# Optimization experiments

Measured on AMD Instinct MI355X. Metric: run time of the kernel, lower is better.

## Reference

```python
import jax, jax.numpy as jnp
import numpy as np
import math

B, S, D, H = 2, 1024, 4096, 32
HD = D // H          # head_dim = 128
P = 10               # prompt_len
THETA = 500000.0     # rope_theta


def _rope(t, cos, sin):
    # t: [b, s, h, hd]; pairs (2i, 2i+1) form complex numbers as in view_as_complex
    tr = t[..., 0::2]
    ti = t[..., 1::2]
    c = cos[None, :, None, :]
    s = sin[None, :, None, :]
    out = jnp.stack([tr * c - ti * s, tr * s + ti * c], axis=-1)  # [b,s,h,hd/2,2]
    return out.reshape(t.shape)


def setup_inputs() -> dict:
    key = jax.random.key(0)
    ks = jax.random.split(key, 8)
    sc = 0.02
    x = jax.random.normal(ks[0], (B, S, D), jnp.float32)
    wq = jax.random.normal(ks[1], (D, D), jnp.float32) * sc
    wk = jax.random.normal(ks[2], (D, D), jnp.float32) * sc
    wv = jax.random.normal(ks[3], (D, D), jnp.float32) * sc
    wo = jax.random.normal(ks[4], (D, D), jnp.float32) * sc
    prompt = jax.random.normal(ks[5], (P, D), jnp.float32)
    prompt_gate = jax.random.normal(ks[6], (1, H, 1, 1), jnp.float32) * 0.1
    # RoPE tables (real/imag of freqs_cis)
    inv = 1.0 / (THETA ** (jnp.arange(0, HD, 2, dtype=jnp.float32) / HD))  # [HD/2]
    ang = jnp.outer(jnp.arange(S, dtype=jnp.float32), inv)                 # [S, HD/2]
    freqs_cos = jnp.cos(ang)
    freqs_sin = jnp.sin(ang)
    # causal additive mask
    mask = jnp.triu(jnp.full((S, S), -1e9, jnp.float32), 1)[None, None]
    type_weight = jax.random.uniform(ks[7], (B, S, 1), jnp.float32)
    return dict(x=x, wq=wq, wk=wk, wv=wv, wo=wo, prompt=prompt,
                prompt_gate=prompt_gate, freqs_cos=freqs_cos,
                freqs_sin=freqs_sin, mask=mask, type_weight=type_weight,
                start_pos=0)


def reference(x, wq, wk, wv, wo, prompt, prompt_gate, freqs_cos, freqs_sin,
              mask, type_weight, start_pos):
    # training-mode forward: start_pos == 0, keys/values = current tokens
    scale = 1.0 / math.sqrt(HD)
    xq = (x @ wq.T).reshape(B, S, H, HD)
    xk = (x @ wk.T).reshape(B, S, H, HD)
    xv = (x @ wv.T).reshape(B, S, H, HD)
    xq = _rope(xq, freqs_cos, freqs_sin)
    xk = _rope(xk, freqs_cos, freqs_sin)
    q = xq.transpose(0, 2, 1, 3)  # [b,h,s,hd]
    k = xk.transpose(0, 2, 1, 3)
    v = xv.transpose(0, 2, 1, 3)
    scores = jnp.einsum('bhqd,bhkd->bhqk', q, k) * scale + mask
    probs = jax.nn.softmax(scores, axis=-1)
    out = jnp.einsum('bhqk,bhkd->bhqd', probs, v)  # [b,h,s,hd]
    # gated prompt injection (num_experts == 1); type_weight unused, as in source
    pk = (prompt @ wk.T).reshape(P, H, HD)
    pv = (prompt @ wv.T).reshape(P, H, HD)
    p_scores = jnp.einsum('bhqd,phd->bhqp', q, pk) * scale
    p_probs = prompt_gate * jax.nn.softmax(p_scores, axis=-1)
    p_out = jnp.einsum('bhqp,phd->bhqd', p_probs, pv)
    out = (out + p_out).transpose(0, 2, 1, 3).reshape(B, S, D)
    return out @ wo.T
```

## Files before the change

### kernel.cpp

```cpp
#include <hip/hip_runtime.h>
#include <hip/hip_bf16.h>
#include <stdint.h>

typedef __hip_bfloat16 bf16;
typedef __attribute__((ext_vector_type(8))) short short8;
typedef __attribute__((ext_vector_type(4))) float f32x4;

#define SCALE_ 0.08838834764831845f

static __device__ __forceinline__ float bf2f(short u) {
  unsigned int x = ((unsigned int)(unsigned short)u) << 16;
  return __builtin_bit_cast(float, x);
}
static __device__ __forceinline__ short f2bf(float f) {
  __hip_bfloat16 h = __float2bfloat16(f);
  return __builtin_bit_cast(short, h);
}
static __device__ __forceinline__ f32x4 mfma16(short8 a, short8 b, f32x4 c) {
  return __builtin_amdgcn_mfma_f32_16x16x32_bf16(a, b, c, 0, 0, 0);
}
static __device__ __forceinline__ void gl_lds16(const bf16* g, bf16* l) {
  __builtin_amdgcn_global_load_lds(
      (const __attribute__((address_space(1))) unsigned int*)g,
      (__attribute__((address_space(3))) unsigned int*)l, 16, 0, 0);
}

__global__ __launch_bounds__(256) void cvt6(
    const float* __restrict__ sx, const float* __restrict__ sq,
    const float* __restrict__ sk, const float* __restrict__ sv,
    const float* __restrict__ so, const float* __restrict__ sp,
    bf16* __restrict__ dx, bf16* __restrict__ dq, bf16* __restrict__ dk,
    bf16* __restrict__ dv, bf16* __restrict__ d4, bf16* __restrict__ dp)
{
  int b = blockIdx.x;
  const float* s; bf16* d; int off;
  if (b < 4096)       { s = sx; d = dx; off = b; }
  else if (b < 12288) { s = sq; d = dq; off = b - 4096; }
  else if (b < 20480) { s = sk; d = dk; off = b - 12288; }
  else if (b < 28672) { s = sv; d = dv; off = b - 20480; }
  else if (b < 36864) { s = so; d = d4; off = b - 28672; }
  else                { s = sp; d = dp; off = b - 36864; }
  long base = (long)off * 2048 + threadIdx.x * 8;
  f32x4 a = *(const f32x4*)(s + base);
  f32x4 c = *(const f32x4*)(s + base + 4);
  short8 o;
#pragma unroll
  for (int j = 0; j < 4; j++) { o[j] = f2bf(a[j]); o[4 + j] = f2bf(c[j]); }
  *(short8*)(d + base) = o;
}

template <int NKT, bool KSPLIT>
__global__ __launch_bounds__(512, 2) void gemm_bt(
    const bf16* __restrict__ A, const bf16* __restrict__ A2,
    const bf16* __restrict__ B0, const bf16* __restrict__ B1, const bf16* __restrict__ B2w,
    bf16* __restrict__ C0, bf16* __restrict__ C1, bf16* __restrict__ C2,
    bf16* __restrict__ P1, bf16* __restrict__ P2,
    float* __restrict__ CF,
    int M1, int Mtot)
{
  __shared__ char lds[131072];
  const int tid = threadIdx.x, w = tid >> 6, l = tid & 63;
  const int lr = l & 15, lg = l >> 4;
  const int wm = w >> 2, wn = w & 3;
  const int z = blockIdx.z;
  const bf16* Bw = KSPLIT ? B0 : ((z == 0) ? B0 : ((z == 1) ? B1 : B2w));
  bf16* C  = (z == 0) ? C0 : ((z == 1) ? C1 : C2);
  bf16* Cp = (KSPLIT || z == 0) ? (bf16*)0 : ((z == 1) ? P1 : P2);
  float* CFz = CF;
  long koff = 0;
  if (KSPLIT) { koff = (long)z * NKT * 64; CFz = CF + (long)z * M1 * 4096; }

  const int cpx = gridDim.x >> 3, orig = blockIdx.x;
  const int wg = (orig & 7) * cpx + (orig >> 3);
  const long m0 = (long)(wg >> 4) * 256;
  const long n0 = (long)(wg & 15) * 256;

  const int r0 = ((tid >> 3) << 1) | ((tid >> 2) & 1);
  const int c0 = (tid & 3) ^ ((tid >> 3) & 3);
  const bf16 *pa0, *pa1;
  {
    long mx = (long)(Mtot - M1) - 1;
    long g0 = m0 + r0, g1 = m0 + r0 + 128;
    const bf16 *q0, *q1;
    if (g0 < M1) q0 = A + g0 * 4096;
    else { long rr = g0 - M1; if (rr > mx) rr = mx; q0 = A2 + rr * 4096; }
    if (g1 < M1) q1 = A + g1 * 4096;
    else { long rr = g1 - M1; if (rr > mx) rr = mx; q1 = A2 + rr * 4096; }
    pa0 = q0 + c0 * 8 + koff;
    pa1 = q1 + c0 * 8 + koff;
  }
  const bf16* pb0 = Bw + (n0 + r0) * 4096 + c0 * 8 + koff;
  const bf16* pb1 = pb0 + (long)128 * 4096;

  const int ro  = (lr >> 1) * 128 + (((lr & 1) * 4) + (lg ^ ((lr >> 1) & 3))) * 16;
  const int aro = wm * 8192 + ro;
  const int bro = wn * 4096 + ro;

  f32x4 acc[8][4];
#pragma unroll
  for (int i = 0; i < 8; i++)
#pragma unroll
    for (int j = 0; j < 4; j++) acc[i][j] = (f32x4){0.f, 0.f, 0.f, 0.f};

  short8 af[4], bf[4];

#define STGA(S_, KE_)                                                        \
  {                                                                          \
    bf16* d_ = (bf16*)(lds + (S_) * 16384) + tid * 8;                        \
    gl_lds16(pa0 + (KE_), d_);                                               \
    gl_lds16(pa1 + (KE_), d_ + 4096);                                        \
  }
#define STGB(S_, KE_)                                                        \
  {                                                                          \
    bf16* d_ = (bf16*)(lds + (S_) * 16384) + tid * 8;                        \
    gl_lds16(pb0 + (KE_), d_);                                               \
    gl_lds16(pb1 + (KE_), d_ + 4096);                                        \
  }
#define SYNC(VM_)                                                            \
  {                                                                          \
    asm volatile("s_waitcnt vmcnt(" VM_ ")" ::: "memory");                   \
    __builtin_amdgcn_s_barrier();                                            \
    __builtin_amdgcn_sched_barrier(0);                                       \
  }
#define PHASE(PRB_, AU_, BU_, MO_, LB_, STG_)                                \
  {                                                                          \
    STG_                                                                     \
    const char* ab_ = lds + (PRB_) + (AU_) + aro;                            \
    _Pragma("unroll") for (int mi = 0; mi < 4; mi++)                         \
      af[mi] = *(const short8*)(ab_ + ((MO_) + mi) * 1024);                  \
    if (LB_) {                                                               \
      const char* bb_ = lds + (PRB_) + (BU_) + bro;                          \
      _Pragma("unroll") for (int ni = 0; ni < 4; ni++)                       \
        bf[ni] = *(const short8*)(bb_ + ni * 1024);                          \
    }                                                                        \
    asm volatile("s_waitcnt lgkmcnt(0)" ::: "memory");                       \
    __builtin_amdgcn_sched_barrier(0);                                       \
    __builtin_amdgcn_s_setprio(1);                                           \
    _Pragma("unroll") for (int mi = 0; mi < 4; mi++)                         \
      _Pragma("unroll") for (int ni = 0; ni < 4; ni++)                       \
        acc[(MO_) + mi][ni] = mfma16(af[mi], bf[ni], acc[(MO_) + mi][ni]);   \
    __builtin_amdgcn_s_setprio(0);                                           \
  }
#define KT(PRB_, S6_, S7_, S8_, S9_, KE1_, KE2_)                             \
  SYNC("8") PHASE(PRB_, 0, 16384, 0, 1, STGA(S6_, KE1_))                     \
  PHASE(PRB_, 0, 16384, 4, 0, STGB(S7_, KE1_))                               \
  SYNC("8") PHASE(PRB_, 32768, 49152, 0, 1, STGA(S8_, KE2_))                 \
  PHASE(PRB_, 32768, 49152, 4, 0, STGB(S9_, KE2_))

  STGA(0, 0) STGB(1, 0) STGA(2, 32) STGB(3, 32) STGA(4, 64) STGB(5, 64)

  for (int t = 0; t < NKT - 2; t += 2) {
    const int ka = (t + 1) * 64 + 32, kb = (t + 2) * 64;
    const int kc = (t + 2) * 64 + 32, kd = (t + 3) * 64;
    KT(0, 6, 7, 0, 1, ka, kb)
    KT(65536, 2, 3, 4, 5, kc, kd)
  }
  {
    const int kel = (NKT - 1) * 64 + 32;
    SYNC("8") PHASE(0, 0, 16384, 0, 1, STGA(6, kel))
    PHASE(0, 0, 16384, 4, 0, STGB(7, kel))
    SYNC("8") PHASE(0, 32768, 49152, 0, 1, )
    PHASE(0, 32768, 49152, 4, 0, )
  }
  SYNC("4") PHASE(65536, 0, 16384, 0, 1, )
  PHASE(65536, 0, 16384, 4, 0, )
  SYNC("0") PHASE(65536, 32768, 49152, 0, 1, )
  PHASE(65536, 32768, 49152, 4, 0, )

#undef KT
#undef PHASE
#undef SYNC
#undef STGB
#undef STGA

#pragma unroll
  for (int mi = 0; mi < 8; mi++) {
#pragma unroll
    for (int ni = 0; ni < 4; ni++) {
      long col = n0 + wn * 64 + ni * 16 + lr;
      f32x4 v = acc[mi][ni];
#pragma unroll
      for (int j = 0; j < 4; j++) {
        long row = m0 + wm * 128 + mi * 16 + lg * 4 + j;
        if (CFz) {
          CFz[row * 4096 + col] = v[j];
        } else if (row < M1) {
          *(short*)(C + row * 4096 + col) = f2bf(v[j]);
        } else if (Cp != 0 && row < Mtot) {
          *(short*)(Cp + (row - M1) * 4096 + col) = f2bf(v[j]);
        }
      }
    }
  }
}

__global__ __launch_bounds__(512, 2) void gemm_n128(
    const bf16* __restrict__ A, const bf16* __restrict__ Bw,
    float* __restrict__ CF)
{
  __shared__ char lds[98304];
  const int tid = threadIdx.x, w = tid >> 6, l = tid & 63;
  const int lr = l & 15, lg = l >> 4;
  const int wm = w >> 1, wn = w & 1;

  const int cpx = gridDim.x >> 3, orig = blockIdx.x;
  const int wg = (orig & 7) * cpx + (orig >> 3);
  const long m0 = (long)(wg >> 5) * 256;
  const long n0 = (long)(wg & 31) * 128;

  const int r0 = ((tid >> 3) << 1) | ((tid >> 2) & 1);
  const int c0 = (tid & 3) ^ ((tid >> 3) & 3);
  const bf16* pa0 = A + (m0 + r0) * 4096 + c0 * 8;
  const bf16* pa1 = pa0 + (long)128 * 4096;
  const bf16* pb0 = Bw + (n0 + r0) * 4096 + c0 * 8;

  const int ro  = (lr >> 1) * 128 + (((lr & 1) * 4) + (lg ^ ((lr >> 1) & 3))) * 16;
  const int aro = wm * 4096 + ro;
  const int bro = wn * 4096 + ro;

  f32x4 acc[4][4];
#pragma unroll
  for (int i = 0; i < 4; i++)
#pragma unroll
    for (int j = 0; j < 4; j++) acc[i][j] = (f32x4){0.f, 0.f, 0.f, 0.f};

  short8 af[4], bf[4];

#define NSTGA(SB_, KE_)                                                      \
  {                                                                          \
    bf16* d_ = (bf16*)(lds + (SB_)) + tid * 8;                               \
    gl_lds16(pa0 + (KE_), d_);                                               \
    gl_lds16(pa1 + (KE_), d_ + 4096);                                        \
  }
#define NSTGB(SB_, KE_)                                                      \
  {                                                                          \
    bf16* d_ = (bf16*)(lds + (SB_)) + tid * 8;                               \
    gl_lds16(pb0 + (KE_), d_);                                               \
  }
#define NSYNC(VM_)                                                           \
  {                                                                          \
    asm volatile("s_waitcnt vmcnt(" VM_ ")" ::: "memory");                   \
    __builtin_amdgcn_s_barrier();                                            \
    __builtin_amdgcn_sched_barrier(0);                                       \
  }
#define NPH(PRB_, AO_, BO_, STG_)                                            \
  {                                                                          \
    STG_                                                                     \
    const char* ab_ = lds + (PRB_) + (AO_) + aro;                            \
    _Pragma("unroll") for (int mi = 0; mi < 4; mi++)                         \
      af[mi] = *(const short8*)(ab_ + mi * 1024);                            \
    const char* bb_ = lds + (PRB_) + (BO_) + bro;                            \
    _Pragma("unroll") for (int ni = 0; ni < 4; ni++)                         \
      bf[ni] = *(const short8*)(bb_ + ni * 1024);                            \
    asm volatile("s_waitcnt lgkmcnt(0)" ::: "memory");                       \
    __builtin_amdgcn_sched_barrier(0);                                       \
    __builtin_amdgcn_s_setprio(1);                                           \
    _Pragma("unroll") for (int mi = 0; mi < 4; mi++)                         \
      _Pragma("unroll") for (int ni = 0; ni < 4; ni++)                       \
        acc[mi][ni] = mfma16(af[mi], bf[ni], acc[mi][ni]);                   \
    __builtin_amdgcn_s_setprio(0);                                           \
  }

  NSTGA(0, 0)      NSTGB(16384, 0)
  NSTGA(24576, 32) NSTGB(40960, 32)
  NSTGA(49152, 64) NSTGB(65536, 64)

  for (int t = 0; t < 62; t += 2) {
    const int ka = (t + 1) * 64 + 32;
    const int kb = (t + 2) * 64;
    NSYNC("3") NPH(0, 0, 16384,     NSTGA(49152 + 24576, ka) NSTGB(49152 + 40960, ka))
    NSYNC("3") NPH(0, 24576, 40960, NSTGA(0, kb) NSTGB(16384, kb))
    const int kc = (t + 2) * 64 + 32;
    const int kd = (t + 3) * 64;
    NSYNC("3") NPH(49152, 0, 16384,     NSTGA(24576, kc) NSTGB(40960, kc))
    NSYNC("3") NPH(49152, 24576, 40960, NSTGA(49152, kd) NSTGB(49152 + 16384, kd))
  }
  NSYNC("3") NPH(0, 0, 16384,     NSTGA(49152 + 24576, 63 * 64 + 32) NSTGB(49152 + 40960, 63 * 64 + 32))
  NSYNC("3") NPH(0, 24576, 40960, )
  NSYNC("3") NPH(49152, 0, 16384, )
  NSYNC("0") NPH(49152, 24576, 40960, )

#undef NPH
#undef NSYNC
#undef NSTGB
#undef NSTGA

#pragma unroll
  for (int mi = 0; mi < 4; mi++) {
#pragma unroll
    for (int ni = 0; ni < 4; ni++) {
      long col = n0 + wn * 64 + ni * 16 + lr;
      f32x4 v = acc[mi][ni];
#pragma unroll
      for (int j = 0; j < 4; j++) {
        long row = m0 + wm * 64 + mi * 16 + lg * 4 + j;
        CF[row * 4096 + col] = v[j];
      }
    }
  }
}

__global__ __launch_bounds__(256) void prep_qkv(
    bf16* __restrict__ Kb,
    const float* __restrict__ FC, const float* __restrict__ FS,
    const bf16* __restrict__ V, bf16* __restrict__ VT)
{
  const int t = threadIdx.x;
  if (blockIdx.y == 0) {
    const int row = blockIdx.x;
    const int s = row & 1023;
    bf16* base = Kb + (long)row * 4096 + t * 16;
    short8 v0 = *(const short8*)base;
    short8 v1 = *(const short8*)(base + 8);
    const float* cp = FC + s * 64 + (t & 7) * 8;
    const float* sp = FS + s * 64 + (t & 7) * 8;
    f32x4 c0 = *(const f32x4*)cp;
    f32x4 c1 = *(const f32x4*)(cp + 4);
    f32x4 s0 = *(const f32x4*)sp;
    f32x4 s1 = *(const f32x4*)(sp + 4);
    short8 o0, o1;
#pragma unroll
    for (int j = 0; j < 4; j++) {
      float c = c0[j], sn = s0[j];
      float e = bf2f(v0[2 * j]), od = bf2f(v0[2 * j + 1]);
      o0[2 * j] = f2bf(e * c - od * sn);
      o0[2 * j + 1] = f2bf(e * sn + od * c);
      float c2 = c1[j], sn2 = s1[j];
      float e2 = bf2f(v1[2 * j]), od2 = bf2f(v1[2 * j + 1]);
      o1[2 * j] = f2bf(e2 * c2 - od2 * sn2);
      o1[2 * j + 1] = f2bf(e2 * sn2 + od2 * c2);
    }
    *(short8*)base = o0;
    *(short8*)(base + 8) = o1;
    return;
  }
  if (blockIdx.x >= 1024) return;
  __shared__ bf16 T[64 * 128];
  const int st = (blockIdx.x & 15) * 64, bh = blockIdx.x >> 4;
  const int b = bh >> 5, h = bh & 31;
  const bf16* src = V + ((long)(b * 1024 + st)) * 4096 + h * 128;
#pragma unroll
  for (int rr = 0; rr < 4; ++rr) {
    int i = t + rr * 256;
    int s_l = i >> 4, c = i & 15;
    short8 v = *(const short8*)(src + (long)s_l * 4096 + c * 8);
    *(short8*)((char*)T + s_l * 256 + ((c ^ (s_l & 7)) * 16)) = v;
  }
  __syncthreads();
#pragma unroll
  for (int rr = 0; rr < 4; ++rr) {
    int i = t + rr * 256;
    int d = i >> 3, cs = i & 7;
    short8 ov;
#pragma unroll
    for (int e = 0; e < 8; e++) {
      int s_l = cs * 8 + e;
      ov[e] = *(const short*)((char*)T + s_l * 256 + (((d >> 3) ^ (s_l & 7)) * 16) + (d & 7) * 2);
    }
    *(short8*)(VT + ((long)bh * 128 + d) * 1024 + st + cs * 8) = ov;
  }
}

__global__ __launch_bounds__(256) void flash_attn(
    const bf16* __restrict__ Q, const bf16* __restrict__ Kg, const bf16* __restrict__ VT,
    const bf16* __restrict__ PK, const bf16* __restrict__ PV,
    const float* __restrict__ GATE, const float* __restrict__ FC,
    const float* __restrict__ FS, bf16* __restrict__ O)
{
  __shared__ bf16 Kl[2][64 * 128];
  __shared__ bf16 Vl[2][128 * 64];
  __shared__ bf16 PKl[16 * 128];
  __shared__ bf16 PVl[128 * 16];
  __shared__ bf16 Pl[4][16 * 64];
  const int tid = threadIdx.x, w = tid >> 6, l = tid & 63;
  const int lg = l >> 4, lr = l & 15;
  const int qb = blockIdx.x, bh = blockIdx.y;
  const int b = bh >> 5, h = bh & 31;
  const int q0 = qb * 64 + w * 16;

  short8 qf[4];
  {
    const bf16* qp = Q + ((long)(b * 1024 + q0 + lr)) * 4096 + h * 128 + lg * 8;
    const int s = q0 + lr;
#pragma unroll
    for (int c = 0; c < 4; c++) {
      short8 v = *(const short8*)(qp + c * 32);
      f32x4 fc = *(const f32x4*)(FC + s * 64 + c * 16 + lg * 4);
      f32x4 fs = *(const f32x4*)(FS + s * 64 + c * 16 + lg * 4);
#pragma unroll
      for (int j = 0; j < 4; j++) {
        float e = bf2f(v[2 * j]), od = bf2f(v[2 * j + 1]);
        v[2 * j] = f2bf(e * fc[j] - od * fs[j]);
        v[2 * j + 1] = f2bf(e * fs[j] + od * fc[j]);
      }
      qf[c] = v;
    }
  }
  {
    int rowp = tid >> 4, pc = tid & 15, lc = pc ^ (rowp & 7);
    short8 v = {0, 0, 0, 0, 0, 0, 0, 0};
    if (rowp < 10) v = *(const short8*)(PK + (long)rowp * 4096 + h * 128 + lc * 8);
    *(short8*)((char*)PKl + tid * 16) = v;
  }
  {
    int d = tid >> 1, pb = (tid & 1) * 8;
#pragma unroll
    for (int e = 0; e < 8; e++) {
      int p = pb + e;
      short v = 0;
      if (p < 10) v = __builtin_bit_cast(short, PV[(long)p * 4096 + h * 128 + d]);
      *(short*)((char*)PVl + d * 32 + (((p >> 3) ^ (d & 1)) * 16) + (p & 7) * 2) = v;
    }
  }
  const float gate = GATE[h];

  f32x4 o[8];
#pragma unroll
  for (int i = 0; i < 8; i++) o[i] = (f32x4){0.f, 0.f, 0.f, 0.f};
  float m_[4] = {-1e30f, -1e30f, -1e30f, -1e30f};
  float l_[4] = {0.f, 0.f, 0.f, 0.f};

  const int nt = qb + 1;
  const bf16* Kbase = Kg + ((long)b * 1024) * 4096 + h * 128;
  const bf16* Vbase = VT + ((long)bh) * 128 * 1024;
  bf16* pw = &Pl[w][0];

#define FSTG(BUF_, J_)                                                        \
  {                                                                           \
    _Pragma("unroll") for (int r_ = 0; r_ < 4; ++r_) {                        \
      int i_ = tid + 256 * r_;                                                \
      int kr_ = i_ >> 4, kc_ = (i_ & 15) ^ (kr_ & 7);                         \
      gl_lds16(Kbase + (long)((J_) * 64 + kr_) * 4096 + kc_ * 8,              \
               &Kl[BUF_][0] + i_ * 8);                                        \
      int vd_ = i_ >> 3, vc_ = (i_ & 7) ^ (vd_ & 7);                          \
      gl_lds16(Vbase + (long)vd_ * 1024 + (J_) * 64 + vc_ * 8,                \
               &Vl[BUF_][0] + i_ * 8);                                        \
    }                                                                         \
  }

  FSTG(0, 0)
  for (int j = 0; j < nt; ++j) {
    __builtin_amdgcn_s_barrier();
    if (j + 1 < nt) {
      FSTG((j + 1) & 1, j + 1)
      asm volatile("s_waitcnt vmcnt(8)" ::: "memory");
    } else {
      asm volatile("s_waitcnt vmcnt(0)" ::: "memory");
    }
    __builtin_amdgcn_s_barrier();
    __builtin_amdgcn_sched_barrier(0);

    const char* kb = (const char*)&Kl[j & 1][0];
    const char* vb = (const char*)&Vl[j & 1][0];

    f32x4 s[4];
#pragma unroll
    for (int ns = 0; ns < 4; ns++) {
      f32x4 a = (f32x4){0.f, 0.f, 0.f, 0.f};
      int krow = ns * 16 + lr;
      int sw = krow & 7;
#pragma unroll
      for (int c = 0; c < 4; c++) {
        short8 kf = *(const short8*)(kb + krow * 256 + (((c * 4 + lg) ^ sw) * 16));
        a = mfma16(qf[c], kf, a);
      }
      int key = j * 64 + krow;
#pragma unroll
      for (int r = 0; r < 4; r++) {
        int qr = q0 + lg * 4 + r;
        s[ns][r] = a[r] * SCALE_ + ((key <= qr) ? 0.0f : -1e30f);
      }
    }
    float mx[4], cor[4], sum[4];
#pragma unroll
    for (int r = 0; r < 4; r++)
      mx[r] = fmaxf(fmaxf(s[0][r], s[1][r]), fmaxf(s[2][r], s[3][r]));
#pragma unroll
    for (int xm = 1; xm < 16; xm <<= 1)
#pragma unroll
      for (int r = 0; r < 4; r++) mx[r] = fmaxf(mx[r], __shfl_xor(mx[r], xm, 64));
#pragma unroll
    for (int r = 0; r < 4; r++) {
      float mn = fmaxf(m_[r], mx[r]);
      cor[r] = __expf(m_[r] - mn);
      m_[r] = mn;
      sum[r] = 0.f;
    }
#pragma unroll
    for (int ns = 0; ns < 4; ns++)
#pragma unroll
      for (int r = 0; r < 4; r++) {
        s[ns][r] = __expf(s[ns][r] - m_[r]);
        sum[r] += s[ns][r];
      }
#pragma unroll
    for (int xm = 1; xm < 16; xm <<= 1)
#pragma unroll
      for (int r = 0; r < 4; r++) sum[r] += __shfl_xor(sum[r], xm, 64);
#pragma unroll
    for (int r = 0; r < 4; r++) l_[r] = l_[r] * cor[r] + sum[r];
#pragma unroll
    for (int df = 0; df < 8; df++)
#pragma unroll
      for (int r = 0; r < 4; r++) o[df][r] *= cor[r];

#pragma unroll
    for (int ns = 0; ns < 4; ns++)
#pragma unroll
      for (int r = 0; r < 4; r++) {
        int row = lg * 4 + r;
        int ch = ns * 2 + (lr >> 3);
        *(short*)((char*)pw + row * 128 + ((ch ^ (row & 7)) * 16) + (lr & 7) * 2)
            = f2bf(s[ns][r]);
      }
    asm volatile("s_waitcnt lgkmcnt(0)" ::: "memory");
    __builtin_amdgcn_sched_barrier(0);
    short8 pf0 = *(const short8*)((char*)pw + lr * 128 + ((lg ^ (lr & 7)) * 16));
    short8 pf1 = *(const short8*)((char*)pw + lr * 128 + (((4 + lg) ^ (lr & 7)) * 16));

#pragma unroll
    for (int df = 0; df < 8; df++) {
      int d = df * 16 + lr;
      short8 vf0 = *(const short8*)(vb + d * 128 + ((lg ^ (d & 7)) * 16));
      short8 vf1 = *(const short8*)(vb + d * 128 + (((4 + lg) ^ (d & 7)) * 16));
      o[df] = mfma16(pf0, vf0, o[df]);
      o[df] = mfma16(pf1, vf1, o[df]);
    }
  }
#undef FSTG

  f32x4 ps;
  {
    f32x4 a = (f32x4){0.f, 0.f, 0.f, 0.f};
    const char* kp = (const char*)PKl + lr * 256;
    int sw = lr & 7;
#pragma unroll
    for (int c = 0; c < 4; c++) {
      short8 kf = *(const short8*)(kp + (((c * 4 + lg) ^ sw) * 16));
      a = mfma16(qf[c], kf, a);
    }
#pragma unroll
    for (int r = 0; r < 4; r++) ps[r] = (lr < 10) ? a[r] * SCALE_ : -1e30f;
  }
  {
    float pm[4], pss[4];
#pragma unroll
    for (int r = 0; r < 4; r++) pm[r] = ps[r];
#pragma unroll
    for (int xm = 1; xm < 16; xm <<= 1)
#pragma unroll
      for (int r = 0; r < 4; r++) pm[r] = fmaxf(pm[r], __shfl_xor(pm[r], xm, 64));
#pragma unroll
    for (int r = 0; r < 4; r++) { ps[r] = __expf(ps[r] - pm[r]); pss[r] = ps[r]; }
#pragma unroll
    for (int xm = 1; xm < 16; xm <<= 1)
#pragma unroll
      for (int r = 0; r < 4; r++) pss[r] += __shfl_xor(pss[r], xm, 64);
#pragma unroll
    for (int r = 0; r < 4; r++) ps[r] = ps[r] / pss[r];
  }
#pragma unroll
  for (int r = 0; r < 4; r++) {
    int row = lg * 4 + r;
    int ch0 = (lr >> 3);
    *(short*)((char*)pw + row * 128 + ((ch0 ^ (row & 7)) * 16) + (lr & 7) * 2) = f2bf(ps[r]);
    int ch1 = 2 + (lr >> 3);
    *(short*)((char*)pw + row * 128 + ((ch1 ^ (row & 7)) * 16) + (lr & 7) * 2) = 0;
  }
  asm volatile("s_waitcnt lgkmcnt(0)" ::: "memory");
  __builtin_amdgcn_sched_barrier(0);
  short8 pf2 = *(const short8*)((char*)pw + lr * 128 + ((lg ^ (lr & 7)) * 16));
  f32x4 po[8];
#pragma unroll
  for (int df = 0; df < 8; df++) {
    int d = df * 16 + lr;
    short8 vf = {0, 0, 0, 0, 0, 0, 0, 0};
    if (lg < 2) vf = *(const short8*)((const char*)PVl + d * 32 + ((lg ^ (d & 1)) * 16));
    po[df] = mfma16(pf2, vf, (f32x4){0.f, 0.f, 0.f, 0.f});
  }

  bf16* op = O + ((long)(b * 1024 + q0 + lg * 4)) * 4096 + h * 128 + lr;
#pragma unroll
  for (int df = 0; df < 8; df++)
#pragma unroll
    for (int r = 0; r < 4; r++) {
      float val = o[df][r] / l_[r] + gate * po[df][r];
      *(short*)(op + (long)r * 4096 + df * 16) = f2bf(val);
    }
}

extern "C" void kernel_launch(void* const* d_in, const int* in_sizes, int n_in,
                              void* d_out, int out_size, void* d_ws, size_t ws_size,
                              hipStream_t stream) {
  (void)in_sizes; (void)n_in; (void)out_size; (void)ws_size;
  const float* x      = (const float*)d_in[0];
  const float* wq     = (const float*)d_in[1];
  const float* wk     = (const float*)d_in[2];
  const float* wv     = (const float*)d_in[3];
  const float* wo     = (const float*)d_in[4];
  const float* prompt = (const float*)d_in[5];
  const float* gate   = (const float*)d_in[6];
  const float* fcos   = (const float*)d_in[7];
  const float* fsin   = (const float*)d_in[8];
  float* out = (float*)d_out;
  char* ws = (char*)d_ws;

  size_t o = 0;
  bf16* xb  = (bf16*)(ws + o); o += (size_t)8388608 * 2;
  bf16* wqb = (bf16*)(ws + o); o += (size_t)16777216 * 2;
  bf16* wkb = (bf16*)(ws + o); o += (size_t)16777216 * 2;
  bf16* wvb = (bf16*)(ws + o); o += (size_t)16777216 * 2;
  bf16* wob = (bf16*)(ws + o); o += (size_t)16777216 * 2;
  bf16* pb  = (bf16*)(ws + o); o += (size_t)40960 * 2;
  bf16* q_ws  = (bf16*)(ws + o); o += (size_t)2048 * 4096 * 2;
  bf16* k_ws  = (bf16*)(ws + o); o += (size_t)2048 * 4096 * 2;
  bf16* v_ws  = (bf16*)(ws + o); o += (size_t)2048 * 4096 * 2;
  bf16* vT_ws = (bf16*)(ws + o); o += (size_t)2048 * 4096 * 2;
  bf16* pk_ws = (bf16*)(ws + o); o += (size_t)40960 * 2;
  bf16* pv_ws = (bf16*)(ws + o); o += (size_t)40960 * 2;
  bf16* attn_ws = v_ws;

  cvt6<<<dim3(36884), 256, 0, stream>>>(x, wq, wk, wv, wo, prompt,
                                        xb, wqb, wkb, wvb, wob, pb);
  gemm_bt<64, false><<<dim3(144, 1, 3), 512, 0, stream>>>(
      xb, pb, wqb, wkb, wvb, q_ws, k_ws, v_ws, pk_ws, pv_ws, (float*)0, 2048, 2058);
  prep_qkv<<<dim3(2048, 2), 256, 0, stream>>>(k_ws, fcos, fsin, v_ws, vT_ws);
  flash_attn<<<dim3(16, 64), 256, 0, stream>>>(
      q_ws, k_ws, vT_ws, pk_ws, pv_ws, gate, fcos, fsin, attn_ws);
  gemm_n128<<<dim3(256), 512, 0, stream>>>(attn_ws, wob, out);
}
```

Measured before the change: 477.5 us.

## Double-buffer register fragments in QKV GEMM to overlap LDS reads with MFMA

Rewrites the QKV projection GEMM main loop so LDS fragment reads for the next phase are issued before the MFMAs of the current phase, using two register sets (afA/afB, bfA/bfB) and partial lgkmcnt waits. It also removes the unused K-split template path and adds s_setprio raises around the MFMA sections in flash attention. The aim is to hide LDS read latency behind matrix instructions. In exchange it raises register pressure and relies on fragile hand-counted waitcnt values for correctness.

```diff
diff --git a/kernel.cpp b/kernel.cpp
--- a/kernel.cpp
+++ b/kernel.cpp
@@ -49,13 +49,11 @@
   *(short8*)(d + base) = o;
 }
 
-template <int NKT, bool KSPLIT>
 __global__ __launch_bounds__(512, 2) void gemm_bt(
     const bf16* __restrict__ A, const bf16* __restrict__ A2,
     const bf16* __restrict__ B0, const bf16* __restrict__ B1, const bf16* __restrict__ B2w,
     bf16* __restrict__ C0, bf16* __restrict__ C1, bf16* __restrict__ C2,
     bf16* __restrict__ P1, bf16* __restrict__ P2,
-    float* __restrict__ CF,
     int M1, int Mtot)
 {
   __shared__ char lds[131072];
@@ -63,12 +61,9 @@
   const int lr = l & 15, lg = l >> 4;
   const int wm = w >> 2, wn = w & 3;
   const int z = blockIdx.z;
-  const bf16* Bw = KSPLIT ? B0 : ((z == 0) ? B0 : ((z == 1) ? B1 : B2w));
+  const bf16* Bw = (z == 0) ? B0 : ((z == 1) ? B1 : B2w);
   bf16* C  = (z == 0) ? C0 : ((z == 1) ? C1 : C2);
-  bf16* Cp = (KSPLIT || z == 0) ? (bf16*)0 : ((z == 1) ? P1 : P2);
-  float* CFz = CF;
-  long koff = 0;
-  if (KSPLIT) { koff = (long)z * NKT * 64; CFz = CF + (long)z * M1 * 4096; }
+  bf16* Cp = (z == 0) ? (bf16*)0 : ((z == 1) ? P1 : P2);
 
   const int cpx = gridDim.x >> 3, orig = blockIdx.x;
   const int wg = (orig & 7) * cpx + (orig >> 3);
@@ -86,10 +81,10 @@
     else { long rr = g0 - M1; if (rr > mx) rr = mx; q0 = A2 + rr * 4096; }
     if (g1 < M1) q1 = A + g1 * 4096;
     else { long rr = g1 - M1; if (rr > mx) rr = mx; q1 = A2 + rr * 4096; }
-    pa0 = q0 + c0 * 8 + koff;
-    pa1 = q1 + c0 * 8 + koff;
-  }
-  const bf16* pb0 = Bw + (n0 + r0) * 4096 + c0 * 8 + koff;
+    pa0 = q0 + c0 * 8;
+    pa1 = q1 + c0 * 8;
+  }
+  const bf16* pb0 = Bw + (n0 + r0) * 4096 + c0 * 8;
   const bf16* pb1 = pb0 + (long)128 * 4096;
 
   const int ro  = (lr >> 1) * 128 + (((lr & 1) * 4) + (lg ^ ((lr >> 1) & 3))) * 16;
@@ -102,76 +97,74 @@
 #pragma unroll
     for (int j = 0; j < 4; j++) acc[i][j] = (f32x4){0.f, 0.f, 0.f, 0.f};
 
-  short8 af[4], bf[4];
-
-#define STGA(S_, KE_)                                                        \
+  short8 afA[4], afB[4], bfA[4], bfB[4];
+
+#define SGA(BASE_, KE_)                                                      \
   {                                                                          \
-    bf16* d_ = (bf16*)(lds + (S_) * 16384) + tid * 8;                        \
+    bf16* d_ = (bf16*)(lds + (BASE_)) + tid * 8;                             \
     gl_lds16(pa0 + (KE_), d_);                                               \
     gl_lds16(pa1 + (KE_), d_ + 4096);                                        \
   }
-#define STGB(S_, KE_)                                                        \
+#define SGB(BASE_, KE_)                                                      \
   {                                                                          \
-    bf16* d_ = (bf16*)(lds + (S_) * 16384) + tid * 8;                        \
+    bf16* d_ = (bf16*)(lds + (BASE_)) + tid * 8;                             \
     gl_lds16(pb0 + (KE_), d_);                                               \
     gl_lds16(pb1 + (KE_), d_ + 4096);                                        \
   }
-#define SYNC(VM_)                                                            \
-  {                                                                          \
-    asm volatile("s_waitcnt vmcnt(" VM_ ")" ::: "memory");                   \
-    __builtin_amdgcn_s_barrier();                                            \
-    __builtin_amdgcn_sched_barrier(0);                                       \
-  }
-#define PHASE(PRB_, AU_, BU_, MO_, LB_, STG_)                                \
-  {                                                                          \
-    STG_                                                                     \
-    const char* ab_ = lds + (PRB_) + (AU_) + aro;                            \
-    _Pragma("unroll") for (int mi = 0; mi < 4; mi++)                         \
-      af[mi] = *(const short8*)(ab_ + ((MO_) + mi) * 1024);                  \
-    if (LB_) {                                                               \
-      const char* bb_ = lds + (PRB_) + (BU_) + bro;                          \
-      _Pragma("unroll") for (int ni = 0; ni < 4; ni++)                       \
-        bf[ni] = *(const short8*)(bb_ + ni * 1024);                          \
-    }                                                                        \
-    asm volatile("s_waitcnt lgkmcnt(0)" ::: "memory");                       \
-    __builtin_amdgcn_sched_barrier(0);                                       \
-    __builtin_amdgcn_s_setprio(1);                                           \
-    _Pragma("unroll") for (int mi = 0; mi < 4; mi++)                         \
-      _Pragma("unroll") for (int ni = 0; ni < 4; ni++)                       \
-        acc[(MO_) + mi][ni] = mfma16(af[mi], bf[ni], acc[(MO_) + mi][ni]);   \
-    __builtin_amdgcn_s_setprio(0);                                           \
-  }
-#define KT(PRB_, S6_, S7_, S8_, S9_, KE1_, KE2_)                             \
-  SYNC("8") PHASE(PRB_, 0, 16384, 0, 1, STGA(S6_, KE1_))                     \
-  PHASE(PRB_, 0, 16384, 4, 0, STGB(S7_, KE1_))                               \
-  SYNC("8") PHASE(PRB_, 32768, 49152, 0, 1, STGA(S8_, KE2_))                 \
-  PHASE(PRB_, 32768, 49152, 4, 0, STGB(S9_, KE2_))
-
-  STGA(0, 0) STGB(1, 0) STGA(2, 32) STGB(3, 32) STGA(4, 64) STGB(5, 64)
-
-  for (int t = 0; t < NKT - 2; t += 2) {
+#define RDA(SET_, BASE_, MO_)                                                \
+  _Pragma("unroll") for (int mi = 0; mi < 4; mi++)                           \
+    SET_[mi] = *(const short8*)(lds + (BASE_) + aro + ((MO_) + mi) * 1024);
+#define RDB(SET_, BASE_)                                                     \
+  _Pragma("unroll") for (int ni = 0; ni < 4; ni++)                           \
+    SET_[ni] = *(const short8*)(lds + (BASE_) + bro + ni * 1024);
+#define VMC(N_) asm volatile("s_waitcnt vmcnt(" N_ ")" ::: "memory");
+#define WAITK(N_)                                                            \
+  asm volatile("s_waitcnt lgkmcnt(" N_ ")" ::: "memory");                    \
+  __builtin_amdgcn_sched_barrier(0);                                         \
+  __builtin_amdgcn_s_barrier();                                              \
+  __builtin_amdgcn_sched_barrier(0);
+#define MM(AF_, BF_, MO_)                                                    \
+  __builtin_amdgcn_s_setprio(1);                                             \
+  _Pragma("unroll") for (int mi = 0; mi < 4; mi++)                           \
+    _Pragma("unroll") for (int ni = 0; ni < 4; ni++)                         \
+      acc[(MO_) + mi][ni] = mfma16(AF_[mi], BF_[ni], acc[(MO_) + mi][ni]);   \
+  __builtin_amdgcn_s_setprio(0);
+
+  SGA(0, 0) SGB(16384, 0) SGA(32768, 32) SGB(49152, 32)
+  SGA(65536, 64) SGB(65536 + 16384, 64)
+  VMC("8")
+  __builtin_amdgcn_s_barrier();
+  __builtin_amdgcn_sched_barrier(0);
+  RDA(afA, 0, 0) RDB(bfA, 16384)
+
+  for (int t = 0; t < 62; t += 2) {
     const int ka = (t + 1) * 64 + 32, kb = (t + 2) * 64;
     const int kc = (t + 2) * 64 + 32, kd = (t + 3) * 64;
-    KT(0, 6, 7, 0, 1, ka, kb)
-    KT(65536, 2, 3, 4, 5, kc, kd)
-  }
-  {
-    const int kel = (NKT - 1) * 64 + 32;
-    SYNC("8") PHASE(0, 0, 16384, 0, 1, STGA(6, kel))
-    PHASE(0, 0, 16384, 4, 0, STGB(7, kel))
-    SYNC("8") PHASE(0, 32768, 49152, 0, 1, )
-    PHASE(0, 32768, 49152, 4, 0, )
-  }
-  SYNC("4") PHASE(65536, 0, 16384, 0, 1, )
-  PHASE(65536, 0, 16384, 4, 0, )
-  SYNC("0") PHASE(65536, 32768, 49152, 0, 1, )
-  PHASE(65536, 32768, 49152, 4, 0, )
-
-#undef KT
-#undef PHASE
-#undef SYNC
-#undef STGB
-#undef STGA
+    SGA(65536 + 32768, ka) RDA(afB, 0, 4)                              WAITK("4") MM(afA, bfA, 0)
+    SGB(65536 + 49152, ka) VMC("8") RDA(afA, 32768, 0) RDB(bfB, 49152) WAITK("8") MM(afB, bfA, 4)
+    SGA(0, kb)             RDA(afB, 32768, 4)                          WAITK("4") MM(afA, bfB, 0)
+    SGB(16384, kb)         VMC("8") RDA(afA, 65536, 0) RDB(bfA, 65536 + 16384) WAITK("8") MM(afB, bfB, 4)
+    SGA(32768, kc)         RDA(afB, 65536, 4)                          WAITK("4") MM(afA, bfA, 0)
+    SGB(49152, kc)         VMC("8") RDA(afA, 65536 + 32768, 0) RDB(bfB, 65536 + 49152) WAITK("8") MM(afB, bfA, 4)
+    SGA(65536, kd)         RDA(afB, 65536 + 32768, 4)                  WAITK("4") MM(afA, bfB, 0)
+    SGB(65536 + 16384, kd) VMC("8") RDA(afA, 0, 0) RDB(bfA, 16384)     WAITK("8") MM(afB, bfB, 4)
+  }
+  SGA(65536 + 32768, 4064) RDA(afB, 0, 4)                              WAITK("4") MM(afA, bfA, 0)
+  SGB(65536 + 49152, 4064) VMC("8") RDA(afA, 32768, 0) RDB(bfB, 49152) WAITK("8") MM(afB, bfA, 4)
+  RDA(afB, 32768, 4)                                                   WAITK("4") MM(afA, bfB, 0)
+  VMC("4") RDA(afA, 65536, 0) RDB(bfA, 65536 + 16384)                  WAITK("8") MM(afB, bfB, 4)
+  RDA(afB, 65536, 4)                                                   WAITK("4") MM(afA, bfA, 0)
+  VMC("0") RDA(afA, 65536 + 32768, 0) RDB(bfB, 65536 + 49152)          WAITK("8") MM(afB, bfA, 4)
+  RDA(afB, 65536 + 32768, 4)                                           WAITK("4") MM(afA, bfB, 0)
+  WAITK("0") MM(afB, bfB, 4)
+
+#undef MM
+#undef WAITK
+#undef VMC
+#undef RDB
+#undef RDA
+#undef SGB
+#undef SGA
 
 #pragma unroll
   for (int mi = 0; mi < 8; mi++) {
@@ -182,9 +175,7 @@
 #pragma unroll
       for (int j = 0; j < 4; j++) {
         long row = m0 + wm * 128 + mi * 16 + lg * 4 + j;
-        if (CFz) {
-          CFz[row * 4096 + col] = v[j];
-        } else if (row < M1) {
+        if (row < M1) {
           *(short*)(C + row * 4096 + col) = f2bf(v[j]);
         } else if (Cp != 0 && row < Mtot) {
           *(short*)(Cp + (row - M1) * 4096 + col) = f2bf(v[j]);
@@ -454,6 +445,7 @@
     const char* vb = (const char*)&Vl[j & 1][0];
 
     f32x4 s[4];
+    __builtin_amdgcn_s_setprio(1);
 #pragma unroll
     for (int ns = 0; ns < 4; ns++) {
       f32x4 a = (f32x4){0.f, 0.f, 0.f, 0.f};
@@ -471,6 +463,7 @@
         s[ns][r] = a[r] * SCALE_ + ((key <= qr) ? 0.0f : -1e30f);
       }
     }
+    __builtin_amdgcn_s_setprio(0);
     float mx[4], cor[4], sum[4];
 #pragma unroll
     for (int r = 0; r < 4; r++)
@@ -518,6 +511,7 @@
     short8 pf0 = *(const short8*)((char*)pw + lr * 128 + ((lg ^ (lr & 7)) * 16));
     short8 pf1 = *(const short8*)((char*)pw + lr * 128 + (((4 + lg) ^ (lr & 7)) * 16));
 
+    __builtin_amdgcn_s_setprio(1);
 #pragma unroll
     for (int df = 0; df < 8; df++) {
       int d = df * 16 + lr;
@@ -526,6 +520,7 @@
       o[df] = mfma16(pf0, vf0, o[df]);
       o[df] = mfma16(pf1, vf1, o[df]);
     }
+    __builtin_amdgcn_s_setprio(0);
   }
 #undef FSTG
 
@@ -622,8 +617,8 @@
 
   cvt6<<<dim3(36884), 256, 0, stream>>>(x, wq, wk, wv, wo, prompt,
                                         xb, wqb, wkb, wvb, wob, pb);
-  gemm_bt<64, false><<<dim3(144, 1, 3), 512, 0, stream>>>(
-      xb, pb, wqb, wkb, wvb, q_ws, k_ws, v_ws, pk_ws, pv_ws, (float*)0, 2048, 2058);
+  gemm_bt<<<dim3(144, 1, 3), 512, 0, stream>>>(
+      xb, pb, wqb, wkb, wvb, q_ws, k_ws, v_ws, pk_ws, pv_ws, 2048, 2058);
   prep_qkv<<<dim3(2048, 2), 256, 0, stream>>>(k_ws, fcos, fsin, v_ws, vT_ws);
   flash_attn<<<dim3(16, 64), 256, 0, stream>>>(
       q_ws, k_ws, vT_ws, pk_ws, pv_ws, gate, fcos, fsin, attn_ws);
```

Result: no change. 482.4 us (+1.0%).
